# Kernel tuning notes

Measured on AMD Instinct MI355X. Metric: run time of the kernel, lower is better.

Reference implementation:

```python
import jax, jax.numpy as jnp
import numpy as np

S, B, E, H = 1024, 4, 1024, 16
D = E // H  # head_dim = 64


def setup_inputs() -> dict:
    key = jax.random.key(0)
    ks = jax.random.split(key, 22)
    inp = {}
    names_io = ["query_r", "query_i", "key_r", "key_i", "value_r", "value_i"]
    for i, n in enumerate(names_io):
        inp[n] = jax.random.normal(ks[i], (S, B, E), dtype=jnp.float32)
    scale = 0.02
    j = 6
    for p in ["q", "k", "v", "o"]:
        inp[f"w{p}_r"] = jax.random.normal(ks[j], (E, E), dtype=jnp.float32) * scale; j += 1
        inp[f"w{p}_i"] = jax.random.normal(ks[j], (E, E), dtype=jnp.float32) * scale; j += 1
        inp[f"b{p}_r"] = jax.random.normal(ks[j], (E,), dtype=jnp.float32) * scale; j += 1
        inp[f"b{p}_i"] = jax.random.normal(ks[j], (E,), dtype=jnp.float32) * scale; j += 1
    return inp


def _clinear(x, wr, wi, br, bi):
    # complex linear: x @ W^T + b, torch Linear convention (weight [out,in])
    w = wr + 1j * wi
    b = br + 1j * bi
    return x @ w.T + b


def reference(query_r, query_i, key_r, key_i, value_r, value_i,
              wq_r, wq_i, bq_r, bq_i, wk_r, wk_i, bk_r, bk_i,
              wv_r, wv_i, bv_r, bv_i, wo_r, wo_i, bo_r, bo_i):
    # batch_first=False: inputs are [S, B, E] -> [B, S, E]
    q = jnp.transpose(query_r + 1j * query_i, (1, 0, 2))
    k = jnp.transpose(key_r + 1j * key_i, (1, 0, 2))
    v = jnp.transpose(value_r + 1j * value_i, (1, 0, 2))

    def heads(x):  # [B,S,E] -> [B,H,S,D]
        return jnp.transpose(x.reshape(B, S, H, D), (0, 2, 1, 3))

    Q = heads(_clinear(q, wq_r, wq_i, bq_r, bq_i))
    K = heads(_clinear(k, wk_r, wk_i, bk_r, bk_i))
    V = heads(_clinear(v, wv_r, wv_i, bv_r, bv_i))

    scores = jnp.einsum("bhqd,bhkd->bhqk", Q, K) / jnp.sqrt(jnp.float32(D))
    # split softmax: softmax over real and imag parts independently
    attn = (jax.nn.softmax(scores.real, axis=-1)
            + 1j * jax.nn.softmax(scores.imag, axis=-1))
    out = jnp.einsum("bhqk,bhkd->bhqd", attn, V)  # [B,H,S,D]
    out = jnp.transpose(out, (0, 2, 1, 3)).reshape(B, S, E)
    out = _clinear(out, wo_r, wo_i, bo_r, bo_i)
    out = jnp.transpose(out, (1, 0, 2))  # back to [S,B,E]
    # return complex output as stacked (real, imag) floats: [S,B,E,2]
    return jnp.stack([out.real, out.imag], axis=-1)
```

## Files before the change

kernel.cpp:

```cpp
#include <hip/hip_runtime.h>
#include <hip/hip_bf16.h>
#include <stdint.h>

#define S_LEN 1024
#define B_SZ  4
#define E_SZ  1024
#define H_CNT 16
#define D_HD  64
#define N1    (B_SZ * H_CNT * S_LEN * D_HD)
#define WELEM (E_SZ * E_SZ)

typedef __attribute__((ext_vector_type(8))) short short8;
typedef __attribute__((ext_vector_type(4))) float f32x4;

__device__ __forceinline__ ushort f2bf(float f) {
  union { float f; uint32_t u; } v; v.f = f;
  uint32_t u = v.u;
  uint32_t r = (u + 0x7fffu + ((u >> 16) & 1u)) >> 16;
  return (ushort)r;
}
__device__ __forceinline__ float bf2f(ushort u) {
  union { uint32_t u; float f; } v; v.u = ((uint32_t)u) << 16;
  return v.f;
}
__device__ __forceinline__ short8 pack8(float4 a, float4 b) {
  short8 r;
  r[0] = (short)f2bf(a.x); r[1] = (short)f2bf(a.y);
  r[2] = (short)f2bf(a.z); r[3] = (short)f2bf(a.w);
  r[4] = (short)f2bf(b.x); r[5] = (short)f2bf(b.y);
  r[6] = (short)f2bf(b.z); r[7] = (short)f2bf(b.w);
  return r;
}
static __device__ __forceinline__ f32x4 mfma16(short8 a, short8 b, f32x4 c) {
  return __builtin_amdgcn_mfma_f32_16x16x32_bf16(a, b, c, 0, 0, 0);
}

typedef const __attribute__((address_space(1))) void gv_t;
typedef __attribute__((address_space(3))) void lv_t;
__device__ __forceinline__ void gld16(const void* g, void* l) {
  __builtin_amdgcn_global_load_lds((gv_t*)g, (lv_t*)l, 16, 0, 0);
}

__global__ __launch_bounds__(256) void cast_w8(
    const float* __restrict__ s0, const float* __restrict__ s1,
    const float* __restrict__ s2, const float* __restrict__ s3,
    const float* __restrict__ s4, const float* __restrict__ s5,
    const float* __restrict__ s6, const float* __restrict__ s7,
    ushort* __restrict__ dst)
{
  const size_t i = (size_t)blockIdx.x * blockDim.x + threadIdx.x;
  const size_t e = i * 4;
  const int which = (int)(e >> 20);
  const size_t off = e & (WELEM - 1);
  const float* s = which < 4
      ? (which < 2 ? (which == 0 ? s0 : s1) : (which == 2 ? s2 : s3))
      : (which < 6 ? (which == 4 ? s4 : s5) : (which == 6 ? s6 : s7));
  const float4 f = *(const float4*)(s + off);
  ushort4 u;
  u.x = f2bf(f.x); u.y = f2bf(f.y); u.z = f2bf(f.z); u.w = f2bf(f.w);
  *(ushort4*)(dst + e) = u;
}

__global__ __launch_bounds__(256) void castA(
    const float* __restrict__ xr, const float* __restrict__ xi,
    ushort* __restrict__ yr, ushort* __restrict__ yi)
{
  const size_t e = ((size_t)blockIdx.x * 256 + threadIdx.x) * 8;
  float4 a = *(const float4*)(xr + e);
  float4 b = *(const float4*)(xr + e + 4);
  *(short8*)(yr + e) = pack8(a, b);
  a = *(const float4*)(xi + e);
  b = *(const float4*)(xi + e + 4);
  *(short8*)(yi + e) = pack8(a, b);
}

template<int MODE>
__global__ __launch_bounds__(256) void cgemm(
    const ushort* __restrict__ ar_, const ushort* __restrict__ ai_,
    const ushort* __restrict__ wre, const ushort* __restrict__ wim,
    const float* __restrict__ bre, const float* __restrict__ bim,
    ushort* __restrict__ yr, ushort* __restrict__ yi,
    float* __restrict__ outf, float scale)
{
  __shared__ __align__(16) ushort sAr[128 * 64], sAi[128 * 64];
  __shared__ __align__(16) ushort sBr[64 * 64],  sBi[64 * 64];

  const int tid  = threadIdx.x;
  const int lane = tid & 63;
  const int w    = tid >> 6;
  const int wrow = w >> 1, wcol = w & 1;
  const int fr   = lane & 15, fq = lane >> 4;

  const int flat = blockIdx.x + gridDim.x * blockIdx.y;
  const int swz  = (flat & 7) * 64 + (flat >> 3);
  const int n0   = (swz & 15) * 64;
  const int m0   = (swz >> 4) * 128;

  const ushort* gbase = (w == 0) ? ar_ : (w == 1) ? ai_ : (w == 2) ? wre : wim;
  char* sbase = (w == 0) ? (char*)sAr : (w == 1) ? (char*)sAi
              : (w == 2) ? (char*)sBr : (char*)sBi;
  const int rbase = (w < 2) ? m0 : n0;
  const int lrow  = lane >> 3;
  const int sch   = (lane & 7) ^ lrow;
  const ushort* gp0 = gbase + (size_t)(rbase + lrow) * E_SZ + sch * 8;

  f32x4 accR[4][2] = {}, accI[4][2] = {};

  for (int kt = 0; kt < 16; ++kt) {
    const int k0 = kt * 64;
    __syncthreads();
    if (w < 2) {
#pragma unroll
      for (int i = 0; i < 16; ++i)
        gld16(gp0 + (size_t)i * 8 * E_SZ + k0, sbase + i * 1024);
    } else {
#pragma unroll
      for (int i = 0; i < 8; ++i)
        gld16(gp0 + (size_t)i * 8 * E_SZ + k0, sbase + i * 1024);
    }
    __syncthreads();

#pragma unroll
    for (int kk = 0; kk < 2; ++kk) {
      short8 a_r[4], a_i[4], a_n[4], b_r[2], b_i[2];
#pragma unroll
      for (int mi = 0; mi < 4; ++mi) {
        const int row = wrow * 64 + mi * 16 + fr;
        const int off = row * 128 + (((kk * 4 + fq) ^ (row & 7)) << 4);
        a_r[mi] = *(const short8*)((const char*)sAr + off);
        a_i[mi] = *(const short8*)((const char*)sAi + off);
        a_n[mi] = a_i[mi] ^ (short)0x8000;
      }
#pragma unroll
      for (int ni = 0; ni < 2; ++ni) {
        const int row = wcol * 32 + ni * 16 + fr;
        const int off = row * 128 + (((kk * 4 + fq) ^ (row & 7)) << 4);
        b_r[ni] = *(const short8*)((const char*)sBr + off);
        b_i[ni] = *(const short8*)((const char*)sBi + off);
      }
#pragma unroll
      for (int mi = 0; mi < 4; ++mi)
#pragma unroll
        for (int ni = 0; ni < 2; ++ni) {
          accR[mi][ni] = mfma16(a_r[mi], b_r[ni], accR[mi][ni]);
          accR[mi][ni] = mfma16(a_n[mi], b_i[ni], accR[mi][ni]);
          accI[mi][ni] = mfma16(a_r[mi], b_i[ni], accI[mi][ni]);
          accI[mi][ni] = mfma16(a_i[mi], b_r[ni], accI[mi][ni]);
        }
    }
  }

#pragma unroll
  for (int ni = 0; ni < 2; ++ni) {
    const int n = n0 + wcol * 32 + ni * 16 + fr;
    const float bR = bre[n], bI = bim[n];
    const int h = n >> 6, d = n & 63;
#pragma unroll
    for (int mi = 0; mi < 4; ++mi) {
      const int mb = m0 + wrow * 64 + mi * 16 + fq * 4;
#pragma unroll
      for (int q = 0; q < 4; ++q) {
        const int m = mb + q;
        const float vr = (accR[mi][ni][q] + bR) * scale;
        const float vi = (accI[mi][ni][q] + bI) * scale;
        if (MODE == 0) {
          const int s = m >> 2, b = m & 3;
          const size_t o = (((size_t)(b * H_CNT + h) * S_LEN) + s) * D_HD + d;
          yr[o] = f2bf(vr); yi[o] = f2bf(vi);
        } else if (MODE == 1) {
          const int s = m >> 2, b = m & 3;
          const size_t o = (((size_t)(b * H_CNT + h) * D_HD) + d) * S_LEN + s;
          yr[o] = f2bf(vr); yi[o] = f2bf(vi);
        } else {
          const int b = m >> 10, s = m & 1023;
          const size_t o = (((size_t)(s * B_SZ + b) * E_SZ) + n) * 2;
          outf[o] = vr; outf[o + 1] = vi;
        }
      }
    }
  }
}

__global__ __launch_bounds__(256) void cattn_mfma(
    const ushort* __restrict__ Qr, const ushort* __restrict__ Qi,
    const ushort* __restrict__ Kr, const ushort* __restrict__ Ki,
    const ushort* __restrict__ Vtr, const ushort* __restrict__ Vti,
    ushort* __restrict__ AOr, ushort* __restrict__ AOi)
{
  __shared__ __align__(16) ushort sK[2][64][64];
  __shared__ __align__(16) ushort sVt[2][64][64];
  __shared__ __align__(16) ushort sP[4][2][32][64];

  const int tid  = threadIdx.x;
  const int lane = tid & 63;
  const int w    = tid >> 6;
  const int g    = lane >> 4;
  const int fr   = lane & 15;
  const int bh   = blockIdx.y;
  const int b    = bh >> 4, h = bh & 15;
  const int q0   = blockIdx.x * 128;
  const int qw   = q0 + 32 * w;

  short8 qfr[2][2], qfi[2][2];
#pragma unroll
  for (int hq = 0; hq < 2; ++hq) {
    const size_t qrow = ((size_t)bh * S_LEN + qw + hq * 16 + fr) * D_HD;
#pragma unroll
    for (int kk = 0; kk < 2; ++kk) {
      qfr[hq][kk] = *(const short8*)(Qr + qrow + kk * 32 + g * 8);
      qfi[hq][kk] = *(const short8*)(Qi + qrow + kk * 32 + g * 8);
    }
  }

  const int lrow8 = lane >> 3;
  const int sch   = (lane & 7) ^ lrow8;
  const ushort* gsrc; ushort* sdst;
  if      (w == 0) { gsrc = Kr  + (size_t)bh * S_LEN * D_HD; sdst = &sK[0][0][0]; }
  else if (w == 1) { gsrc = Ki  + (size_t)bh * S_LEN * D_HD; sdst = &sK[1][0][0]; }
  else if (w == 2) { gsrc = Vtr + (size_t)bh * D_HD * S_LEN; sdst = &sVt[0][0][0]; }
  else             { gsrc = Vti + (size_t)bh * D_HD * S_LEN; sdst = &sVt[1][0][0]; }
  const bool isK = (w < 2);

  f32x4 accA[2][4] = {}, accAi[2][4] = {}, accB[2][4] = {}, accBi[2][4] = {};
  f32x4 lpr[2] = {}, lpi[2] = {};

  ushort* pR = &sP[w][0][0][0];
  ushort* pI = &sP[w][1][0][0];
  const int par  = fr & 1;
  const int k0b  = fr & ~1;
  ushort* pbuf   = par ? pI : pR;
  const int woff = (k0b * 2) & 15;

  for (int kt = 0; kt < 16; ++kt) {
    __syncthreads();
    if (isK) {
      const ushort* gp = gsrc + (size_t)kt * 4096 + lrow8 * 64 + sch * 8;
#pragma unroll
      for (int i = 0; i < 8; ++i)
        gld16(gp + i * 512, (char*)sdst + i * 1024);
    } else {
      const ushort* gp = gsrc + (size_t)lrow8 * S_LEN + kt * 64 + sch * 8;
#pragma unroll
      for (int i = 0; i < 8; ++i)
        gld16(gp + (size_t)i * 8 * S_LEN, (char*)sdst + i * 1024);
    }
    __syncthreads();

    f32x4 Sr[2][4] = {}, Si[2][4] = {};
#pragma unroll
    for (int n = 0; n < 4; ++n) {
      const int kc = fr + 16 * n;
      const int rb = kc * 128, sw = (kc & 7) << 4;
#pragma unroll
      for (int kk = 0; kk < 2; ++kk) {
        const int off = rb + ((((kk * 4 + g) << 4)) ^ sw);
        short8 krf = *(const short8*)((const char*)&sK[0][0][0] + off);
        short8 kif = *(const short8*)((const char*)&sK[1][0][0] + off);
        short8 kin = kif ^ (short)0x8000;
#pragma unroll
        for (int hq = 0; hq < 2; ++hq) {
          Sr[hq][n] = mfma16(qfr[hq][kk], krf, Sr[hq][n]);
          Sr[hq][n] = mfma16(qfi[hq][kk], kin, Sr[hq][n]);
          Si[hq][n] = mfma16(qfr[hq][kk], kif, Si[hq][n]);
          Si[hq][n] = mfma16(qfi[hq][kk], krf, Si[hq][n]);
        }
      }
    }

#pragma unroll
    for (int hq = 0; hq < 2; ++hq)
#pragma unroll
      for (int n = 0; n < 4; ++n) {
        const int cbase = (k0b + 16 * n) >> 3;
#pragma unroll
        for (int t = 0; t < 4; ++t) {
          float pr = __expf(Sr[hq][n][t]);
          float pi = __expf(Si[hq][n][t]);
          lpr[hq][t] += pr; lpi[hq][t] += pi;
          float pro = __shfl_xor(pr, 1);
          float pio = __shfl_xor(pi, 1);
          float lo = par ? pio : pr;
          float hi = par ? pi  : pro;
          uint32_t pk;
          asm("v_cvt_pk_bf16_f32 %0, %1, %2" : "=v"(pk) : "v"(lo), "v"(hi));
          const int q = hq * 16 + g * 4 + t;
          const int off = q * 128 + ((cbase ^ (q & 7)) << 4) + woff;
          *(uint32_t*)((char*)pbuf + off) = pk;
        }
      }
    asm volatile("s_waitcnt lgkmcnt(0)" ::: "memory");

    short8 prf[2][2], pif[2][2];
#pragma unroll
    for (int hq = 0; hq < 2; ++hq)
#pragma unroll
      for (int kk = 0; kk < 2; ++kk) {
        const int off = (hq * 16 + fr) * 128 + ((((kk * 4 + g) << 4)) ^ ((fr & 7) << 4));
        prf[hq][kk] = *(const short8*)((const char*)pR + off);
        pif[hq][kk] = *(const short8*)((const char*)pI + off);
      }
#pragma unroll
    for (int n = 0; n < 4; ++n) {
      const int d = fr + 16 * n;
      const int rb = d * 128, sw = (d & 7) << 4;
#pragma unroll
      for (int kk = 0; kk < 2; ++kk) {
        const int off = rb + ((((kk * 4 + g) << 4)) ^ sw);
        short8 vrf = *(const short8*)((const char*)&sVt[0][0][0] + off);
        short8 vif = *(const short8*)((const char*)&sVt[1][0][0] + off);
#pragma unroll
        for (int hq = 0; hq < 2; ++hq) {
          accA [hq][n] = mfma16(prf[hq][kk], vrf, accA [hq][n]);
          accAi[hq][n] = mfma16(prf[hq][kk], vif, accAi[hq][n]);
          accB [hq][n] = mfma16(pif[hq][kk], vrf, accB [hq][n]);
          accBi[hq][n] = mfma16(pif[hq][kk], vif, accBi[hq][n]);
        }
      }
    }
  }

#pragma unroll
  for (int mm = 1; mm < 16; mm <<= 1)
#pragma unroll
    for (int hq = 0; hq < 2; ++hq)
#pragma unroll
      for (int t = 0; t < 4; ++t) {
        lpr[hq][t] += __shfl_xor(lpr[hq][t], mm);
        lpi[hq][t] += __shfl_xor(lpi[hq][t], mm);
      }

#pragma unroll
  for (int hq = 0; hq < 2; ++hq) {
    f32x4 ilr, ili;
#pragma unroll
    for (int t = 0; t < 4; ++t) { ilr[t] = 1.f / lpr[hq][t]; ili[t] = 1.f / lpi[hq][t]; }
#pragma unroll
    for (int n = 0; n < 4; ++n) {
      const int e = h * 64 + fr + 16 * n;
#pragma unroll
      for (int t = 0; t < 4; ++t) {
        const int sidx = qw + hq * 16 + g * 4 + t;
        const size_t o = ((size_t)b * S_LEN + sidx) * E_SZ + e;
        AOr[o] = f2bf(accA [hq][n][t] * ilr[t] - accBi[hq][n][t] * ili[t]);
        AOi[o] = f2bf(accAi[hq][n][t] * ilr[t] + accB [hq][n][t] * ili[t]);
      }
    }
  }
}

extern "C" void kernel_launch(void* const* d_in, const int* in_sizes, int n_in,
                              void* d_out, int out_size, void* d_ws, size_t ws_size,
                              hipStream_t stream)
{
    const float* query_r = (const float*)d_in[0];
    const float* query_i = (const float*)d_in[1];
    const float* key_r   = (const float*)d_in[2];
    const float* key_i   = (const float*)d_in[3];
    const float* value_r = (const float*)d_in[4];
    const float* value_i = (const float*)d_in[5];
    const float* wq_r = (const float*)d_in[6];
    const float* wq_i = (const float*)d_in[7];
    const float* bq_r = (const float*)d_in[8];
    const float* bq_i = (const float*)d_in[9];
    const float* wk_r = (const float*)d_in[10];
    const float* wk_i = (const float*)d_in[11];
    const float* bk_r = (const float*)d_in[12];
    const float* bk_i = (const float*)d_in[13];
    const float* wv_r = (const float*)d_in[14];
    const float* wv_i = (const float*)d_in[15];
    const float* bv_r = (const float*)d_in[16];
    const float* bv_i = (const float*)d_in[17];
    const float* wo_r = (const float*)d_in[18];
    const float* wo_i = (const float*)d_in[19];
    const float* bo_r = (const float*)d_in[20];
    const float* bo_i = (const float*)d_in[21];

    ushort* ws   = (ushort*)d_ws;
    ushort* Qr   = ws;
    ushort* Qi   = Qr + (size_t)N1;
    ushort* Kr   = Qi + (size_t)N1;
    ushort* Ki   = Kr + (size_t)N1;
    ushort* Vtr  = Ki + (size_t)N1;
    ushort* Vti  = Vtr + (size_t)N1;
    ushort* Wb   = Vti + (size_t)N1;
    ushort* Wq_r = Wb + 0 * (size_t)WELEM;
    ushort* Wq_i = Wb + 1 * (size_t)WELEM;
    ushort* Wk_r = Wb + 2 * (size_t)WELEM;
    ushort* Wk_i = Wb + 3 * (size_t)WELEM;
    ushort* Wv_r = Wb + 4 * (size_t)WELEM;
    ushort* Wv_i = Wb + 5 * (size_t)WELEM;
    ushort* Wo_r = Wb + 6 * (size_t)WELEM;
    ushort* Wo_i = Wb + 7 * (size_t)WELEM;
    ushort* AOr  = Wb + 8 * (size_t)WELEM;
    ushort* AOi  = AOr + (size_t)N1;

    ushort* Xsr = (ushort*)d_out;
    ushort* Xsi = Xsr + (size_t)N1;

    cast_w8<<<8192, 256, 0, stream>>>(wq_r, wq_i, wk_r, wk_i,
                                      wv_r, wv_i, wo_r, wo_i, Wb);

    dim3 gg(16, 32);

    castA<<<2048, 256, 0, stream>>>(query_r, query_i, Xsr, Xsi);
    cgemm<0><<<gg, 256, 0, stream>>>(Xsr, Xsi, Wq_r, Wq_i, bq_r, bq_i,
                                     Qr, Qi, nullptr, 0.125f);
    castA<<<2048, 256, 0, stream>>>(key_r, key_i, Xsr, Xsi);
    cgemm<0><<<gg, 256, 0, stream>>>(Xsr, Xsi, Wk_r, Wk_i, bk_r, bk_i,
                                     Kr, Ki, nullptr, 1.0f);
    castA<<<2048, 256, 0, stream>>>(value_r, value_i, Xsr, Xsi);
    cgemm<1><<<gg, 256, 0, stream>>>(Xsr, Xsi, Wv_r, Wv_i, bv_r, bv_i,
                                     Vtr, Vti, nullptr, 1.0f);

    cattn_mfma<<<dim3(S_LEN / 128, B_SZ * H_CNT), 256, 0, stream>>>(
        Qr, Qi, Kr, Ki, Vtr, Vti, AOr, AOi);

    cgemm<2><<<gg, 256, 0, stream>>>(AOr, AOi, Wo_r, Wo_i, bo_r, bo_i,
                                     nullptr, nullptr, (float*)d_out, 1.0f);
}
```

Baseline: 309.7 us.

## Prefetch next K tile during PV phase, merge Q/K casts, add MFMA priority

```diff
diff --git a/kernel.cpp b/kernel.cpp
--- a/kernel.cpp
+++ b/kernel.cpp
@@ -61,6 +61,25 @@
   *(ushort4*)(dst + e) = u;
 }
 
+__global__ __launch_bounds__(256) void castA2(
+    const float* __restrict__ xr0, const float* __restrict__ xi0,
+    const float* __restrict__ xr1, const float* __restrict__ xi1,
+    ushort* __restrict__ yr0, ushort* __restrict__ yi0,
+    ushort* __restrict__ yr1, ushort* __restrict__ yi1)
+{
+  int blk = blockIdx.x;
+  const float *xr, *xi; ushort *yr, *yi;
+  if (blk < 2048) { xr = xr0; xi = xi0; yr = yr0; yi = yi0; }
+  else            { xr = xr1; xi = xi1; yr = yr1; yi = yi1; blk -= 2048; }
+  const size_t e = ((size_t)blk * 256 + threadIdx.x) * 8;
+  float4 a = *(const float4*)(xr + e);
+  float4 b = *(const float4*)(xr + e + 4);
+  *(short8*)(yr + e) = pack8(a, b);
+  a = *(const float4*)(xi + e);
+  b = *(const float4*)(xi + e + 4);
+  *(short8*)(yi + e) = pack8(a, b);
+}
+
 __global__ __launch_bounds__(256) void castA(
     const float* __restrict__ xr, const float* __restrict__ xi,
     ushort* __restrict__ yr, ushort* __restrict__ yi)
@@ -138,6 +157,7 @@
         b_r[ni] = *(const short8*)((const char*)sBr + off);
         b_i[ni] = *(const short8*)((const char*)sBi + off);
       }
+      __builtin_amdgcn_s_setprio(1);
 #pragma unroll
       for (int mi = 0; mi < 4; ++mi)
 #pragma unroll
@@ -147,6 +167,7 @@
           accI[mi][ni] = mfma16(a_r[mi], b_i[ni], accI[mi][ni]);
           accI[mi][ni] = mfma16(a_i[mi], b_r[ni], accI[mi][ni]);
         }
+      __builtin_amdgcn_s_setprio(0);
     }
   }
 
@@ -231,22 +252,24 @@
   ushort* pbuf   = par ? pI : pR;
   const int woff = (k0b * 2) & 15;
 
+  if (isK) {
+    const ushort* gp = gsrc + lrow8 * 64 + sch * 8;
+#pragma unroll
+    for (int i = 0; i < 8; ++i)
+      gld16(gp + i * 512, (char*)sdst + i * 1024);
+  }
+  __syncthreads();
+
   for (int kt = 0; kt < 16; ++kt) {
-    __syncthreads();
-    if (isK) {
-      const ushort* gp = gsrc + (size_t)kt * 4096 + lrow8 * 64 + sch * 8;
-#pragma unroll
-      for (int i = 0; i < 8; ++i)
-        gld16(gp + i * 512, (char*)sdst + i * 1024);
-    } else {
+    if (!isK) {
       const ushort* gp = gsrc + (size_t)lrow8 * S_LEN + kt * 64 + sch * 8;
 #pragma unroll
       for (int i = 0; i < 8; ++i)
         gld16(gp + (size_t)i * 8 * S_LEN, (char*)sdst + i * 1024);
     }
-    __syncthreads();
 
     f32x4 Sr[2][4] = {}, Si[2][4] = {};
+    __builtin_amdgcn_s_setprio(1);
 #pragma unroll
     for (int n = 0; n < 4; ++n) {
       const int kc = fr + 16 * n;
@@ -266,6 +289,7 @@
         }
       }
     }
+    __builtin_amdgcn_s_setprio(0);
 
 #pragma unroll
     for (int hq = 0; hq < 2; ++hq)
@@ -288,7 +312,15 @@
           *(uint32_t*)((char*)pbuf + off) = pk;
         }
       }
-    asm volatile("s_waitcnt lgkmcnt(0)" ::: "memory");
+
+    __syncthreads();
+
+    if (isK && kt < 15) {
+      const ushort* gp = gsrc + (size_t)(kt + 1) * 4096 + lrow8 * 64 + sch * 8;
+#pragma unroll
+      for (int i = 0; i < 8; ++i)
+        gld16(gp + i * 512, (char*)sdst + i * 1024);
+    }
 
     short8 prf[2][2], pif[2][2];
 #pragma unroll
@@ -299,6 +331,7 @@
         prf[hq][kk] = *(const short8*)((const char*)pR + off);
         pif[hq][kk] = *(const short8*)((const char*)pI + off);
       }
+    __builtin_amdgcn_s_setprio(1);
 #pragma unroll
     for (int n = 0; n < 4; ++n) {
       const int d = fr + 16 * n;
@@ -317,6 +350,9 @@
         }
       }
     }
+    __builtin_amdgcn_s_setprio(0);
+
+    __syncthreads();
   }
 
 #pragma unroll
@@ -394,22 +430,24 @@
     ushort* AOr  = Wb + 8 * (size_t)WELEM;
     ushort* AOi  = AOr + (size_t)N1;
 
-    ushort* Xsr = (ushort*)d_out;
-    ushort* Xsi = Xsr + (size_t)N1;
+    ushort* Xq_r = (ushort*)d_out;
+    ushort* Xq_i = Xq_r + (size_t)N1;
+    ushort* Xk_r = Xq_i + (size_t)N1;
+    ushort* Xk_i = Xk_r + (size_t)N1;
 
     cast_w8<<<8192, 256, 0, stream>>>(wq_r, wq_i, wk_r, wk_i,
                                       wv_r, wv_i, wo_r, wo_i, Wb);
+    castA2<<<4096, 256, 0, stream>>>(query_r, query_i, key_r, key_i,
+                                     Xq_r, Xq_i, Xk_r, Xk_i);
 
     dim3 gg(16, 32);
 
-    castA<<<2048, 256, 0, stream>>>(query_r, query_i, Xsr, Xsi);
-    cgemm<0><<<gg, 256, 0, stream>>>(Xsr, Xsi, Wq_r, Wq_i, bq_r, bq_i,
+    cgemm<0><<<gg, 256, 0, stream>>>(Xq_r, Xq_i, Wq_r, Wq_i, bq_r, bq_i,
                                      Qr, Qi, nullptr, 0.125f);
-    castA<<<2048, 256, 0, stream>>>(key_r, key_i, Xsr, Xsi);
-    cgemm<0><<<gg, 256, 0, stream>>>(Xsr, Xsi, Wk_r, Wk_i, bk_r, bk_i,
+    cgemm<0><<<gg, 256, 0, stream>>>(Xk_r, Xk_i, Wk_r, Wk_i, bk_r, bk_i,
                                      Kr, Ki, nullptr, 1.0f);
-    castA<<<2048, 256, 0, stream>>>(value_r, value_i, Xsr, Xsi);
-    cgemm<1><<<gg, 256, 0, stream>>>(Xsr, Xsi, Wv_r, Wv_i, bv_r, bv_i,
+    castA<<<2048, 256, 0, stream>>>(value_r, value_i, Xq_r, Xq_i);
+    cgemm<1><<<gg, 256, 0, stream>>>(Xq_r, Xq_i, Wv_r, Wv_i, bv_r, bv_i,
                                      Vtr, Vti, nullptr, 1.0f);
 
     cattn_mfma<<<dim3(S_LEN / 128, B_SZ * H_CNT), 256, 0, stream>>>(
```

Result: slower. 318.7 us (+2.9%).
